# Kernel tuning notes

Measured on AMD Instinct MI355X. Metric: run time of the kernel, lower is better.

The kernel has to match this reference:

```python
import jax, jax.numpy as jnp
import numpy as np

N_NODES = 100000
N_EDGES = 800000
D = 128
N_GRAPHS = 512


def _graph_conv(h, src, dst, norm_src, norm_dst, W, b):
    # DGL GraphConv, norm='both': h' = relu(D_in^{-1/2} * sum_{(u->v)} (D_out^{-1/2} h_u) W + b)
    m = (h * norm_src[:, None])[src]                      # [E, d] gather
    agg = jax.ops.segment_sum(m, dst, num_segments=N_NODES)  # [N, d] scatter-add
    return jax.nn.relu(agg * norm_dst[:, None] @ W + b)


def setup_inputs() -> dict:
    key = jax.random.key(0)
    ks = jax.random.split(key, 10)
    src = jax.random.randint(ks[0], (N_EDGES,), 0, N_NODES)
    dst = jax.random.randint(ks[1], (N_EDGES,), 0, N_NODES)
    graph_ids = jnp.sort(jax.random.randint(ks[2], (N_ODES := N_NODES,), 0, N_GRAPHS))
    features = jax.random.normal(ks[3], (N_NODES, D), dtype=jnp.float32)
    s = 1.0 / np.sqrt(D)
    w1 = jax.random.uniform(ks[4], (D, D), jnp.float32, -s, s)
    b1 = jnp.zeros((D,), jnp.float32)
    w2 = jax.random.uniform(ks[5], (D, D), jnp.float32, -s, s)
    b2 = jnp.zeros((D,), jnp.float32)
    wg = jax.random.uniform(ks[6], (D, 1), jnp.float32, -s, s)
    bg = jnp.zeros((1,), jnp.float32)
    return {"src": src, "dst": dst, "graph_ids": graph_ids, "features": features,
            "w1": w1, "b1": b1, "w2": w2, "b2": b2, "wg": wg, "bg": bg}


def reference(src, dst, graph_ids, features, w1, b1, w2, b2, wg, bg):
    ones = jnp.ones((N_EDGES,), jnp.float32)
    deg_out = jax.ops.segment_sum(ones, src, num_segments=N_NODES)
    deg_in = jax.ops.segment_sum(ones, dst, num_segments=N_NODES)
    norm_src = jax.lax.rsqrt(jnp.maximum(deg_out, 1.0))
    norm_dst = jax.lax.rsqrt(jnp.maximum(deg_in, 1.0))

    h = _graph_conv(features, src, dst, norm_src, norm_dst, w1, b1)
    # dropout is identity in eval mode
    h = _graph_conv(h, src, dst, norm_src, norm_dst, w2, b2)

    # weighted graph aggregation: sigmoid gate per node, per-graph weighted sum
    gate = jax.nn.sigmoid(h @ wg + bg)                    # [N, 1]
    wh = jax.ops.segment_sum(gate * h, graph_ids, num_segments=N_GRAPHS)  # [G, d]
    return wh, h
```

## Files before the change

### kernel.cpp

```cpp
#include <hip/hip_runtime.h>

#define D 128
#define G_GRAPHS 512
#define CCHUNK 8
#define NSLICE 64
#define BINMAX 12544

typedef _Float16 f16;
typedef _Float16 f16x2 __attribute__((ext_vector_type(2)));
typedef _Float16 f16x4 __attribute__((ext_vector_type(4)));
typedef _Float16 f16x8 __attribute__((ext_vector_type(8)));
typedef float f32x4 __attribute__((ext_vector_type(4)));
typedef unsigned short u16;

#define SCAN_CHUNK 2048

__global__ __launch_bounds__(256) void hist_kernel(const int* __restrict__ src, const int* __restrict__ dst,
                                                   u16* __restrict__ pho, u16* __restrict__ phi,
                                                   u16* __restrict__ rank,
                                                   int E, int N, int slice_len, int binsz) {
    __shared__ unsigned hp[BINMAX / 2];
    int c = blockIdx.x, role = blockIdx.y, s = blockIdx.z;
    int c0 = c * binsz;
    int lim = min(binsz, N - c0);
    for (int i = threadIdx.x; i < ((lim + 1) >> 1); i += 256) hp[i] = 0;
    __syncthreads();
    const int* arr = role ? dst : src;
    int e1 = min(E, (s + 1) * slice_len);
    if (role) {
        for (int e = s * slice_len + (int)threadIdx.x; e < e1; e += 256) {
            unsigned v = (unsigned)(arr[e] - c0);
            if (v < (unsigned)lim) {
                unsigned add = (v & 1) ? 0x10000u : 1u;
                unsigned old = atomicAdd(&hp[v >> 1], add);
                rank[e] = (u16)((v & 1) ? (old >> 16) : (old & 0xffffu));
            }
        }
    } else {
        for (int e = s * slice_len + (int)threadIdx.x; e < e1; e += 256) {
            unsigned v = (unsigned)(arr[e] - c0);
            if (v < (unsigned)lim)
                atomicAdd(&hp[v >> 1], (v & 1) ? 0x10000u : 1u);
        }
    }
    __syncthreads();
    u16* outp = (role ? phi : pho) + (size_t)s * N + c0;
    for (int i = threadIdx.x; i < lim; i += 256) {
        unsigned w = hp[i >> 1];
        outp[i] = (u16)((i & 1) ? (w >> 16) : (w & 0xffffu));
    }
}

__global__ void merge_norm_kernel(const u16* __restrict__ pho, u16* __restrict__ phi,
                                  float* __restrict__ norm_src, float* __restrict__ norm_dst,
                                  int* __restrict__ deg_in_total, int N) {
    int n = blockIdx.x * 256 + threadIdx.x;
    if (n >= N) return;
    int so = 0;
    #pragma unroll 8
    for (int s = 0; s < NSLICE; ++s) so += pho[(size_t)s * N + n];
    norm_src[n] = rsqrtf(fmaxf((float)so, 1.0f));
    int run = 0;
    #pragma unroll 8
    for (int s = 0; s < NSLICE; ++s) {
        int v = phi[(size_t)s * N + n];
        phi[(size_t)s * N + n] = (u16)run;
        run += v;
    }
    deg_in_total[n] = run;
    norm_dst[n] = rsqrtf(fmaxf((float)run, 1.0f));
}

__global__ void prescale_kernel(const float* __restrict__ feat, const float* __restrict__ ns,
                                f16x4* __restrict__ out, int count ) {
    int i = blockIdx.x * 256 + threadIdx.x;
    if (i >= count) return;
    float4 v = ((const float4*)feat)[i];
    float s = ns[i >> 5];
    f16x4 o = { (f16)(v.x * s), (f16)(v.y * s), (f16)(v.z * s), (f16)(v.w * s) };
    out[i] = o;
}

__global__ __launch_bounds__(256) void scan1_kernel(const int* __restrict__ deg,
                                                    int* __restrict__ partial,
                                                    int* __restrict__ blocksums, int n) {
    __shared__ int wsum[4];
    int lane = threadIdx.x & 63, wid = threadIdx.x >> 6;
    int base = blockIdx.x * SCAN_CHUNK + (int)threadIdx.x * 8;
    int v[8]; int tsum = 0;
    #pragma unroll
    for (int i = 0; i < 8; ++i) { v[i] = (base + i < n) ? deg[base + i] : 0; tsum += v[i]; }
    int s = tsum;
    #pragma unroll
    for (int off = 1; off < 64; off <<= 1) {
        int t = __shfl_up(s, off);
        if (lane >= off) s += t;
    }
    if (lane == 63) wsum[wid] = s;
    __syncthreads();
    int woff = 0;
    for (int w = 0; w < wid; ++w) woff += wsum[w];
    int run = woff + s - tsum;
    #pragma unroll
    for (int i = 0; i < 8; ++i) {
        if (base + i < n) partial[base + i] = run;
        run += v[i];
    }
    if (threadIdx.x == 255) blocksums[blockIdx.x] = woff + s;
}

__global__ void scan2_kernel(int* __restrict__ bs, int* __restrict__ total_out, int nb) {
    int lane = threadIdx.x;
    int carry = 0;
    for (int base = 0; base < nb; base += 64) {
        int i = base + lane;
        int v = (i < nb) ? bs[i] : 0;
        int s = v;
        #pragma unroll
        for (int off = 1; off < 64; off <<= 1) {
            int t = __shfl_up(s, off);
            if (lane >= off) s += t;
        }
        if (i < nb) bs[i] = carry + s - v;
        carry += __shfl(s, 63);
    }
    if (lane == 0) *total_out = carry;
}

__global__ void scan3_kernel(int* __restrict__ offsets, const int* __restrict__ bs, int n) {
    int i = blockIdx.x * 256 + threadIdx.x;
    if (i >= n) return;
    offsets[i] += bs[i >> 11];
}

__global__ __launch_bounds__(256) void fill_kernel(const int* __restrict__ src, const int* __restrict__ dst,
                                                   const int* __restrict__ offsets, const u16* __restrict__ phi,
                                                   const u16* __restrict__ rank,
                                                   int* __restrict__ csr_src,
                                                   int E, int N, int slice_len) {
    int s = blockIdx.y;
    int e = s * slice_len + blockIdx.x * 256 + threadIdx.x;
    int e1 = min(E, (s + 1) * slice_len);
    if (e >= e1) return;
    int d = dst[e];
    int p = offsets[d] + (int)phi[(size_t)s * N + d] + (int)rank[e];
    csr_src[p] = src[e];
}

__global__ __launch_bounds__(256) void gather_kernel(const f16* __restrict__ x,
                                                     const float* __restrict__ norm_dst,
                                                     const int* __restrict__ offsets,
                                                     const int* __restrict__ csr_src,
                                                     f16* __restrict__ A, int N) {
    int node = __builtin_amdgcn_readfirstlane(blockIdx.x * 4 + ((int)threadIdx.x >> 6));
    int lane = threadIdx.x & 63;
    int g = lane >> 4;
    int l = lane & 15;
    if (node >= N) return;
    int beg = offsets[node], end = offsets[node + 1];
    float acc0[8] = {0.f}, acc1[8] = {0.f};
    int e = beg;
    for (; e + 8 <= end; e += 8) {
        int sa = csr_src[e + g];
        int sb = csr_src[e + 4 + g];
        f16x8 ra = *(const f16x8*)(x + (size_t)sa * D + l * 8);
        f16x8 rb = *(const f16x8*)(x + (size_t)sb * D + l * 8);
        #pragma unroll
        for (int j = 0; j < 8; ++j) { acc0[j] += (float)ra[j]; acc1[j] += (float)rb[j]; }
    }
    if (e + 4 <= end) {
        int sa = csr_src[e + g];
        f16x8 ra = *(const f16x8*)(x + (size_t)sa * D + l * 8);
        #pragma unroll
        for (int j = 0; j < 8; ++j) acc0[j] += (float)ra[j];
        e += 4;
    }
    int rem = end - e;
    if (g < rem) {
        int sa = csr_src[e + g];
        f16x8 ra = *(const f16x8*)(x + (size_t)sa * D + l * 8);
        #pragma unroll
        for (int j = 0; j < 8; ++j) acc1[j] += (float)ra[j];
    }
    float nd = norm_dst[node];
    f16x8 o;
    #pragma unroll
    for (int j = 0; j < 8; ++j) {
        float v = acc0[j] + acc1[j];
        v += __shfl_xor(v, 16);
        v += __shfl_xor(v, 32);
        o[j] = (f16)(v * nd);
    }
    if (g == 0) *(f16x8*)(A + (size_t)node * D + l * 8) = o;
}

template <typename OutT, bool SCALE, bool GATE>
__global__ __launch_bounds__(256) void gemm_kernel(const f16* __restrict__ A,
                                                   const float* __restrict__ Wg,
                                                   const float* __restrict__ bias,
                                                   const float* __restrict__ rowscale,
                                                   const float* __restrict__ wgv,
                                                   const float* __restrict__ bgv,
                                                   float* __restrict__ gate_out,
                                                   OutT* __restrict__ out, int M) {
    __shared__ f16 Wf[4 * 8 * 64 * 8];
    for (int i = threadIdx.x; i < 2048; i += 256) {
        int kg = i >> 7, j = i & 127;
        int k0 = kg * 8;
        f16x8 tmp;
        #pragma unroll
        for (int b = 0; b < 8; ++b) tmp[b] = (f16)Wg[(k0 + b) * D + j];
        int t = k0 >> 5, c = j >> 4;
        int l = ((k0 & 31) >> 3) * 16 + (j & 15);
        *(f16x8*)&Wf[((t * 8 + c) * 64 + l) * 8] = tmp;
    }
    __syncthreads();
    int wave = threadIdx.x >> 6, lane = threadIdx.x & 63;

    for (int row0 = (blockIdx.x * 4 + wave) * 16; row0 < M; row0 += gridDim.x * 64) {
        int arow = row0 + (lane & 15);
        const f16* Abase = A + arow * D + (lane >> 4) * 8;
        f16x8 a[4];
        #pragma unroll
        for (int t = 0; t < 4; ++t) a[t] = *(const f16x8*)(Abase + t * 32);

        float ns[4];
        if (SCALE) {
            #pragma unroll
            for (int r = 0; r < 4; ++r) ns[r] = rowscale[row0 + (lane >> 4) * 4 + r];
        }
        float dotr[4] = {0.f, 0.f, 0.f, 0.f};

        #pragma unroll
        for (int c = 0; c < 8; ++c) {
            f32x4 acc = {0.f, 0.f, 0.f, 0.f};
            #pragma unroll
            for (int t = 0; t < 4; ++t) {
                f16x8 bf = *(const f16x8*)&Wf[((t * 8 + c) * 64 + lane) * 8];
                acc = __builtin_amdgcn_mfma_f32_16x16x32_f16(a[t], bf, acc, 0, 0, 0);
            }
            int col = c * 16 + (lane & 15);
            float bj = bias[col];
            float wgc = GATE ? wgv[col] : 0.f;
            #pragma unroll
            for (int r = 0; r < 4; ++r) {
                int row = row0 + (lane >> 4) * 4 + r;
                float v = fmaxf(acc[r] + bj, 0.f);
                if (SCALE) v *= ns[r];
                out[row * D + col] = (OutT)v;
                if (GATE) dotr[r] += v * wgc;
            }
        }
        if (GATE) {
            float bg0 = bgv[0];
            #pragma unroll
            for (int r = 0; r < 4; ++r) {
                float d = dotr[r];
                d += __shfl_xor(d, 1); d += __shfl_xor(d, 2);
                d += __shfl_xor(d, 4); d += __shfl_xor(d, 8);
                if ((lane & 15) == 0)
                    gate_out[row0 + (lane >> 4) * 4 + r] = 1.0f / (1.0f + __expf(-(d + bg0)));
            }
        }
    }
}

__global__ void gstart_kernel(const int* __restrict__ gid, int* __restrict__ gstart, int N, int G) {
    int n = blockIdx.x * 256 + threadIdx.x;
    if (n >= N) return;
    int g = gid[n];
    if (n == 0) {
        for (int x = 0; x <= g; ++x) gstart[x] = 0;
    } else {
        int pg = gid[n - 1];
        for (int x = pg + 1; x <= g; ++x) gstart[x] = n;
    }
    if (n == N - 1) {
        for (int x = g + 1; x <= G; ++x) gstart[x] = N;
    }
}

__global__ __launch_bounds__(256) void gagg_kernel(const float* __restrict__ h,
                                                   const float* __restrict__ gate,
                                                   const int* __restrict__ gstart,
                                                   float* __restrict__ wh) {
    __shared__ float part[4][D];
    int g = blockIdx.x;
    int wave = threadIdx.x >> 6, lane = threadIdx.x & 63;
    int beg = gstart[g], end = gstart[g + 1];
    float2 acc = {0.f, 0.f};
    for (int n = beg + wave; n < end; n += 4) {
        float gv = gate[n];
        float2 hv = ((const float2*)(h + n * D))[lane];
        acc.x += gv * hv.x;
        acc.y += gv * hv.y;
    }
    part[wave][lane * 2]     = acc.x;
    part[wave][lane * 2 + 1] = acc.y;
    __syncthreads();
    if (wave == 0) {
        float sx = 0.f, sy = 0.f;
        #pragma unroll
        for (int w = 0; w < 4; ++w) { sx += part[w][lane * 2]; sy += part[w][lane * 2 + 1]; }
        float2 o = {sx, sy};
        ((float2*)(wh + g * D))[lane] = o;
    }
}

extern "C" void kernel_launch(void* const* d_in, const int* in_sizes, int n_in,
                              void* d_out, int out_size, void* d_ws, size_t ws_size,
                              hipStream_t stream) {
    const int*   src  = (const int*)d_in[0];
    const int*   dst  = (const int*)d_in[1];
    const int*   gid  = (const int*)d_in[2];
    const float* feat = (const float*)d_in[3];
    const float* w1   = (const float*)d_in[4];
    const float* b1   = (const float*)d_in[5];
    const float* w2   = (const float*)d_in[6];
    const float* b2   = (const float*)d_in[7];
    const float* wg   = (const float*)d_in[8];
    const float* bg   = (const float*)d_in[9];
    int E = in_sizes[0];
    int N = in_sizes[2];
    const int G = G_GRAPHS;

    int binsz     = (N + CCHUNK - 1) / CCHUNK;
    int slice_len = (E + NSLICE - 1) / NSLICE;
    int bps       = (slice_len + 255) / 256;

    char* ws = (char*)d_ws;
    size_t off = 0;
    auto carve = [&](size_t bytes) { void* p = ws + off; off = (off + bytes + 255) & ~(size_t)255; return p; };
    u16*   pho       = (u16*)  carve((size_t)NSLICE * N * 2);
    u16*   phi       = (u16*)  carve((size_t)NSLICE * N * 2);
    u16*   rank      = (u16*)  carve((size_t)E * 2);
    float* norm_src  = (float*)carve((size_t)N * 4);
    float* norm_dst  = (float*)carve((size_t)N * 4);
    int*   deg_in_t  = (int*)  carve((size_t)N * 4);
    int*   offsets   = (int*)  carve((size_t)(N + 1) * 4);
    int*   blocksums = (int*)  carve((size_t)64 * 4);
    int*   csr_src   = (int*)  carve((size_t)E * 4);
    f16*   Xh        = (f16*)  carve((size_t)N * D * 2);
    f16*   A         = (f16*)  carve((size_t)N * D * 2);
    float* gate      = (float*)carve((size_t)N * 4);
    int*   gstart    = (int*)  carve((size_t)(G + 1) * 4);

    float* wh_out = (float*)d_out;
    float* h_out  = (float*)d_out + (size_t)G * D;

    int nb = (N + SCAN_CHUNK - 1) / SCAN_CHUNK;

    dim3 hgrid(CCHUNK, 2, NSLICE);
    hist_kernel<<<hgrid, 256, 0, stream>>>(src, dst, pho, phi, rank, E, N, slice_len, binsz);
    merge_norm_kernel<<<(N + 255) / 256, 256, 0, stream>>>(pho, phi, norm_src, norm_dst, deg_in_t, N);
    prescale_kernel<<<(N * 32 + 255) / 256, 256, 0, stream>>>(feat, norm_src, (f16x4*)Xh, N * 32);

    scan1_kernel<<<nb, 256, 0, stream>>>(deg_in_t, offsets, blocksums, N);
    scan2_kernel<<<1, 64, 0, stream>>>(blocksums, offsets + N, nb);
    scan3_kernel<<<(N + 255) / 256, 256, 0, stream>>>(offsets, blocksums, N);
    dim3 fgrid(bps, NSLICE);
    fill_kernel<<<fgrid, 256, 0, stream>>>(src, dst, offsets, phi, rank, csr_src, E, N, slice_len);

    gather_kernel<<<(N + 3) / 4, 256, 0, stream>>>(Xh, norm_dst, offsets, csr_src, A, N);
    gemm_kernel<f16, true, false><<<512, 256, 0, stream>>>(A, w1, b1, norm_src, nullptr, nullptr, nullptr, Xh, N);
    gather_kernel<<<(N + 3) / 4, 256, 0, stream>>>(Xh, norm_dst, offsets, csr_src, A, N);
    gemm_kernel<float, false, true><<<512, 256, 0, stream>>>(A, w2, b2, nullptr, wg, bg, gate, h_out, N);

    gstart_kernel<<<(N + 255) / 256, 256, 0, stream>>>(gid, gstart, N, G);
    gagg_kernel<<<G, 256, 0, stream>>>(h_out, gate, gstart, wh_out);
}
```

Measured before the change: 214.3 us.

## Fuse neighbor gather into GEMM kernel via LDS staging, halve histogram chunks

The separate gather and GEMM kernels are merged. Each wave gathers and normalizes its 16 destination rows into a padded LDS tile, then runs the MFMA GEMM on it directly, so the intermediate A matrix no longer makes a round trip through global memory and two launches are dropped. The grid now uses one block per 64 rows instead of a fixed 512 blocks, so each block reloads and converts W into LDS, and the gather is done serially per row inside each wave, which may expose more latency. Separately, the histogram uses 4 node chunks with a larger shared bin array, fewer blocks each holding more LDS.

```diff
diff --git a/kernel.cpp b/kernel.cpp
--- a/kernel.cpp
+++ b/kernel.cpp
@@ -2,12 +2,11 @@
 
 #define D 128
 #define G_GRAPHS 512
-#define CCHUNK 8
+#define CCHUNK 4
 #define NSLICE 64
-#define BINMAX 12544
+#define BINMAX 25088
 
 typedef _Float16 f16;
-typedef _Float16 f16x2 __attribute__((ext_vector_type(2)));
 typedef _Float16 f16x4 __attribute__((ext_vector_type(4)));
 typedef _Float16 f16x8 __attribute__((ext_vector_type(8)));
 typedef float f32x4 __attribute__((ext_vector_type(4)));
@@ -147,63 +146,21 @@
     csr_src[p] = src[e];
 }
 
-__global__ __launch_bounds__(256) void gather_kernel(const f16* __restrict__ x,
-                                                     const float* __restrict__ norm_dst,
-                                                     const int* __restrict__ offsets,
-                                                     const int* __restrict__ csr_src,
-                                                     f16* __restrict__ A, int N) {
-    int node = __builtin_amdgcn_readfirstlane(blockIdx.x * 4 + ((int)threadIdx.x >> 6));
-    int lane = threadIdx.x & 63;
-    int g = lane >> 4;
-    int l = lane & 15;
-    if (node >= N) return;
-    int beg = offsets[node], end = offsets[node + 1];
-    float acc0[8] = {0.f}, acc1[8] = {0.f};
-    int e = beg;
-    for (; e + 8 <= end; e += 8) {
-        int sa = csr_src[e + g];
-        int sb = csr_src[e + 4 + g];
-        f16x8 ra = *(const f16x8*)(x + (size_t)sa * D + l * 8);
-        f16x8 rb = *(const f16x8*)(x + (size_t)sb * D + l * 8);
-        #pragma unroll
-        for (int j = 0; j < 8; ++j) { acc0[j] += (float)ra[j]; acc1[j] += (float)rb[j]; }
-    }
-    if (e + 4 <= end) {
-        int sa = csr_src[e + g];
-        f16x8 ra = *(const f16x8*)(x + (size_t)sa * D + l * 8);
-        #pragma unroll
-        for (int j = 0; j < 8; ++j) acc0[j] += (float)ra[j];
-        e += 4;
-    }
-    int rem = end - e;
-    if (g < rem) {
-        int sa = csr_src[e + g];
-        f16x8 ra = *(const f16x8*)(x + (size_t)sa * D + l * 8);
-        #pragma unroll
-        for (int j = 0; j < 8; ++j) acc1[j] += (float)ra[j];
-    }
-    float nd = norm_dst[node];
-    f16x8 o;
-    #pragma unroll
-    for (int j = 0; j < 8; ++j) {
-        float v = acc0[j] + acc1[j];
-        v += __shfl_xor(v, 16);
-        v += __shfl_xor(v, 32);
-        o[j] = (f16)(v * nd);
-    }
-    if (g == 0) *(f16x8*)(A + (size_t)node * D + l * 8) = o;
-}
-
+#define ATPAD 136
 template <typename OutT, bool SCALE, bool GATE>
-__global__ __launch_bounds__(256) void gemm_kernel(const f16* __restrict__ A,
-                                                   const float* __restrict__ Wg,
-                                                   const float* __restrict__ bias,
-                                                   const float* __restrict__ rowscale,
-                                                   const float* __restrict__ wgv,
-                                                   const float* __restrict__ bgv,
-                                                   float* __restrict__ gate_out,
-                                                   OutT* __restrict__ out, int M) {
+__global__ __launch_bounds__(256) void gathergemm_kernel(const f16* __restrict__ x,
+                                                         const float* __restrict__ norm_dst,
+                                                         const int* __restrict__ offsets,
+                                                         const int* __restrict__ csr_src,
+                                                         const float* __restrict__ Wg,
+                                                         const float* __restrict__ bias,
+                                                         const float* __restrict__ rowscale,
+                                                         const float* __restrict__ wgv,
+                                                         const float* __restrict__ bgv,
+                                                         float* __restrict__ gate_out,
+                                                         OutT* __restrict__ out, int M) {
     __shared__ f16 Wf[4 * 8 * 64 * 8];
+    __shared__ f16 At[4][16][ATPAD];
     for (int i = threadIdx.x; i < 2048; i += 256) {
         int kg = i >> 7, j = i & 127;
         int k0 = kg * 8;
@@ -216,18 +173,61 @@
     }
     __syncthreads();
     int wave = threadIdx.x >> 6, lane = threadIdx.x & 63;
+    int g = lane >> 4;
+    int l = lane & 15;
 
     for (int row0 = (blockIdx.x * 4 + wave) * 16; row0 < M; row0 += gridDim.x * 64) {
-        int arow = row0 + (lane & 15);
-        const f16* Abase = A + arow * D + (lane >> 4) * 8;
+        for (int r = 0; r < 16; ++r) {
+            int node = row0 + r;
+            if (node >= M) break;
+            int beg = offsets[node], end = offsets[node + 1];
+            float acc0[8] = {0.f}, acc1[8] = {0.f};
+            int e = beg;
+            for (; e + 8 <= end; e += 8) {
+                int sa = csr_src[e + g];
+                int sb = csr_src[e + 4 + g];
+                f16x8 ra = *(const f16x8*)(x + (size_t)sa * D + l * 8);
+                f16x8 rb = *(const f16x8*)(x + (size_t)sb * D + l * 8);
+                #pragma unroll
+                for (int j = 0; j < 8; ++j) { acc0[j] += (float)ra[j]; acc1[j] += (float)rb[j]; }
+            }
+            if (e + 4 <= end) {
+                int sa = csr_src[e + g];
+                f16x8 ra = *(const f16x8*)(x + (size_t)sa * D + l * 8);
+                #pragma unroll
+                for (int j = 0; j < 8; ++j) acc0[j] += (float)ra[j];
+                e += 4;
+            }
+            int rem = end - e;
+            if (g < rem) {
+                int sa = csr_src[e + g];
+                f16x8 ra = *(const f16x8*)(x + (size_t)sa * D + l * 8);
+                #pragma unroll
+                for (int j = 0; j < 8; ++j) acc1[j] += (float)ra[j];
+            }
+            float nd = norm_dst[node];
+            f16x8 o;
+            #pragma unroll
+            for (int j = 0; j < 8; ++j) {
+                float v = acc0[j] + acc1[j];
+                v += __shfl_xor(v, 16);
+                v += __shfl_xor(v, 32);
+                o[j] = (f16)(v * nd);
+            }
+            if (g == 0) *(f16x8*)&At[wave][r][l * 8] = o;
+        }
+
         f16x8 a[4];
         #pragma unroll
-        for (int t = 0; t < 4; ++t) a[t] = *(const f16x8*)(Abase + t * 32);
+        for (int t = 0; t < 4; ++t) a[t] = *(const f16x8*)&At[wave][l][t * 32 + g * 8];
 
         float ns[4];
         if (SCALE) {
             #pragma unroll
-            for (int r = 0; r < 4; ++r) ns[r] = rowscale[row0 + (lane >> 4) * 4 + r];
+            for (int r = 0; r < 4; ++r) {
+                int row = row0 + g * 4 + r;
+                ns[r] = (row < M) ? rowscale[row] : 0.f;
+            }
         }
         float dotr[4] = {0.f, 0.f, 0.f, 0.f};
 
@@ -239,15 +239,15 @@
                 f16x8 bf = *(const f16x8*)&Wf[((t * 8 + c) * 64 + lane) * 8];
                 acc = __builtin_amdgcn_mfma_f32_16x16x32_f16(a[t], bf, acc, 0, 0, 0);
             }
-            int col = c * 16 + (lane & 15);
+            int col = c * 16 + l;
             float bj = bias[col];
             float wgc = GATE ? wgv[col] : 0.f;
             #pragma unroll
             for (int r = 0; r < 4; ++r) {
-                int row = row0 + (lane >> 4) * 4 + r;
+                int row = row0 + g * 4 + r;
                 float v = fmaxf(acc[r] + bj, 0.f);
                 if (SCALE) v *= ns[r];
-                out[row * D + col] = (OutT)v;
+                if (row < M) out[(size_t)row * D + col] = (OutT)v;
                 if (GATE) dotr[r] += v * wgc;
             }
         }
@@ -255,11 +255,12 @@
             float bg0 = bgv[0];
             #pragma unroll
             for (int r = 0; r < 4; ++r) {
-                float d = dotr[r];
-                d += __shfl_xor(d, 1); d += __shfl_xor(d, 2);
-                d += __shfl_xor(d, 4); d += __shfl_xor(d, 8);
-                if ((lane & 15) == 0)
-                    gate_out[row0 + (lane >> 4) * 4 + r] = 1.0f / (1.0f + __expf(-(d + bg0)));
+                float d2 = dotr[r];
+                d2 += __shfl_xor(d2, 1); d2 += __shfl_xor(d2, 2);
+                d2 += __shfl_xor(d2, 4); d2 += __shfl_xor(d2, 8);
+                int row = row0 + g * 4 + r;
+                if (l == 0 && row < M)
+                    gate_out[row] = 1.0f / (1.0f + __expf(-(d2 + bg0)));
             }
         }
     }
@@ -340,8 +341,8 @@
     int*   offsets   = (int*)  carve((size_t)(N + 1) * 4);
     int*   blocksums = (int*)  carve((size_t)64 * 4);
     int*   csr_src   = (int*)  carve((size_t)E * 4);
-    f16*   Xh        = (f16*)  carve((size_t)N * D * 2);
-    f16*   A         = (f16*)  carve((size_t)N * D * 2);
+    f16*   X1        = (f16*)  carve((size_t)N * D * 2);
+    f16*   X2        = (f16*)  carve((size_t)N * D * 2);
     float* gate      = (float*)carve((size_t)N * 4);
     int*   gstart    = (int*)  carve((size_t)(G + 1) * 4);
 
@@ -353,7 +354,7 @@
     dim3 hgrid(CCHUNK, 2, NSLICE);
     hist_kernel<<<hgrid, 256, 0, stream>>>(src, dst, pho, phi, rank, E, N, slice_len, binsz);
     merge_norm_kernel<<<(N + 255) / 256, 256, 0, stream>>>(pho, phi, norm_src, norm_dst, deg_in_t, N);
-    prescale_kernel<<<(N * 32 + 255) / 256, 256, 0, stream>>>(feat, norm_src, (f16x4*)Xh, N * 32);
+    prescale_kernel<<<(N * 32 + 255) / 256, 256, 0, stream>>>(feat, norm_src, (f16x4*)X1, N * 32);
 
     scan1_kernel<<<nb, 256, 0, stream>>>(deg_in_t, offsets, blocksums, N);
     scan2_kernel<<<1, 64, 0, stream>>>(blocksums, offsets + N, nb);
@@ -361,10 +362,11 @@
     dim3 fgrid(bps, NSLICE);
     fill_kernel<<<fgrid, 256, 0, stream>>>(src, dst, offsets, phi, rank, csr_src, E, N, slice_len);
 
-    gather_kernel<<<(N + 3) / 4, 256, 0, stream>>>(Xh, norm_dst, offsets, csr_src, A, N);
-    gemm_kernel<f16, true, false><<<512, 256, 0, stream>>>(A, w1, b1, norm_src, nullptr, nullptr, nullptr, Xh, N);
-    gather_kernel<<<(N + 3) / 4, 256, 0, stream>>>(Xh, norm_dst, offsets, csr_src, A, N);
-    gemm_kernel<float, false, true><<<512, 256, 0, stream>>>(A, w2, b2, nullptr, wg, bg, gate, h_out, N);
+    int ggrid = (N + 63) / 64;
+    gathergemm_kernel<f16, true, false><<<ggrid, 256, 0, stream>>>(
+        X1, norm_dst, offsets, csr_src, w1, b1, norm_src, nullptr, nullptr, nullptr, X2, N);
+    gathergemm_kernel<float, false, true><<<ggrid, 256, 0, stream>>>(
+        X2, norm_dst, offsets, csr_src, w2, b2, nullptr, wg, bg, gate, h_out, N);
 
     gstart_kernel<<<(N + 255) / 256, 256, 0, stream>>>(gid, gstart, N, G);
     gagg_kernel<<<G, 256, 0, stream>>>(h_out, gate, gstart, wh_out);
```

Result: slower. 391.8 us (+82.8%).
